# Kernel tuning notes

Hardware: AMD Instinct MI355X
Metric: run time of the kernel (lower is better)

Reference implementation:

```python
import jax, jax.numpy as jnp
import numpy as np

NEG_SLOPE = 0.01  # nn.LeakyReLU default

def leaky_relu(v):
    return jnp.where(v >= 0, v, NEG_SLOPE * v)

def setup_inputs() -> dict:
    key = jax.random.key(0)
    ks = jax.random.split(key, 7)
    B, T, I, H, O = 64, 1024, 512, 1024, 512
    x = jax.random.normal(ks[0], (B, T, I), dtype=jnp.float32)
    # Linear params (stored as [in, out] for x @ W + b)
    W_in = jax.random.normal(ks[1], (I, H), dtype=jnp.float32) * (1.0 / np.sqrt(I))
    b_in = jax.random.normal(ks[2], (H,), dtype=jnp.float32) * 0.01
    W_h = jax.random.normal(ks[3], (2 * H, H), dtype=jnp.float32) * (1.0 / np.sqrt(2 * H))
    b_h = jax.random.normal(ks[4], (H,), dtype=jnp.float32) * 0.01
    W_out = jax.random.normal(ks[5], (H, O), dtype=jnp.float32) * (1.0 / np.sqrt(H))
    b_out = jax.random.normal(ks[6], (O,), dtype=jnp.float32) * 0.01
    return {"x": x, "W_in": W_in, "b_in": b_in, "W_h": W_h, "b_h": b_h,
            "W_out": W_out, "b_out": b_out}

def reference(x, W_in, b_in, W_h, b_h, W_out, b_out):
    B, T, I = x.shape
    H = W_in.shape[1]
    # Precompute input projection for all timesteps in one big GEMM:
    # [B,T,I] @ [I,H] -> [B,T,H], then LeakyReLU.
    h_new_all = leaky_relu(jnp.einsum('bti,ih->bth', x, W_in) + b_in)
    h0 = jnp.zeros((B, H), dtype=x.dtype)

    def step(h, h_new_t):
        combined = jnp.concatenate((h_new_t, h), axis=1)  # [B, 2H]
        h_next = leaky_relu(combined @ W_h + b_h)          # [B, H]
        return h_next, None

    # scan over time axis (sequential dependency on h); dropout_rate=0 => identity
    h_final, _ = jax.lax.scan(step, h0, jnp.swapaxes(h_new_all, 0, 1))
    out = h_final @ W_out + b_out  # [B, O]
    return out
```

## Files before the change

kernel.cpp:

```cpp
#include <hip/hip_runtime.h>
#include <hip/hip_bf16.h>

typedef __attribute__((ext_vector_type(8))) short  s16x8;
typedef __attribute__((ext_vector_type(4))) float  f32x4;
typedef __attribute__((ext_vector_type(4))) unsigned short u16x4;
typedef __attribute__((ext_vector_type(4))) unsigned int   u32x4;

#define B_  64
#define T_  1024
#define I_  512
#define H_  1024
#define O_  512
#define MT_ 65536

#define RG_   8
#define CS_   16

__device__ __forceinline__ unsigned short f2bf(float f) {
    unsigned u = __builtin_bit_cast(unsigned, f);
    u += 0x7FFFu + ((u >> 16) & 1u);
    return (unsigned short)(u >> 16);
}
__device__ __forceinline__ float bf2f(unsigned short h) {
    return __builtin_bit_cast(float, ((unsigned)h) << 16);
}
__device__ __forceinline__ void store_out(float* p, float v) { *p = v; }
__device__ __forceinline__ void store_out(unsigned short* p, float v) { *p = f2bf(v); }
__device__ __forceinline__ void store_nt(float* p, float v) {
    asm volatile("global_store_dword %0, %1, off nt" :: "v"(p), "v"(v) : "memory");
}
__device__ __forceinline__ void store_nt(unsigned short* p, float v) {
    unsigned short h = f2bf(v);
    asm volatile("global_store_short %0, %1, off nt" :: "v"(p), "v"(h) : "memory");
}
__device__ __forceinline__ float to_f32(float v) { return v; }
__device__ __forceinline__ float to_f32(unsigned short v) { return bf2f(v); }

template<typename T> struct pre4;
template<> struct pre4<float>          { using t = f32x4; };
template<> struct pre4<unsigned short> { using t = u16x4; };

__device__ __forceinline__ f32x4 pre_ld(const float* p) {
    f32x4 d; asm volatile("global_load_dwordx4 %0, %1, off nt" : "=v"(d) : "v"(p)); return d;
}
__device__ __forceinline__ u16x4 pre_ld(const unsigned short* p) {
    u16x4 d; asm volatile("global_load_dwordx2 %0, %1, off nt" : "=v"(d) : "v"(p)); return d;
}

#define GL2LDS16(gp, lp) __builtin_amdgcn_global_load_lds( \
    (const __attribute__((address_space(1))) void*)(gp),   \
    (__attribute__((address_space(3))) void*)(lp), 16, 0, 0)

__global__ void cvt_x(const float* __restrict__ src, unsigned short* __restrict__ dst, int n) {
    int stride = gridDim.x * blockDim.x * 4;
    for (int i = (blockIdx.x * blockDim.x + threadIdx.x) * 4; i < n; i += stride) {
        const float4 v = *(const float4*)(src + i);
        u16x4 o;
        o.x = f2bf(v.x); o.y = f2bf(v.y); o.z = f2bf(v.z); o.w = f2bf(v.w);
        *(u16x4*)(dst + i) = o;
    }
}

__global__ void cvt_t(const float* __restrict__ src, unsigned short* __restrict__ dst,
                      int SR, int SC, int row_off) {
    __shared__ unsigned short tile[32][33];
    int c0 = blockIdx.x * 32, r0 = blockIdx.y * 32;
    int tx = threadIdx.x, ty = threadIdx.y;
    #pragma unroll
    for (int i = 0; i < 32; i += 8)
        tile[ty + i][tx] = f2bf(src[(size_t)(row_off + r0 + ty + i) * SC + c0 + tx]);
    __syncthreads();
    #pragma unroll
    for (int i = 0; i < 32; i += 8)
        dst[(size_t)(c0 + ty + i) * SR + r0 + tx] = tile[tx][ty + i];
}

__global__ void strip_h(const unsigned* __restrict__ src, unsigned short* __restrict__ dst) {
    int idx = blockIdx.x * blockDim.x + threadIdx.x;
    u32x4 v = *(const u32x4*)(src + idx * 4);
    int rg = idx >> 11, c2 = idx & 2047;
    int q = c2 >> 9, c3 = c2 & 511;
    int j = c3 >> 6, c = c3 & 63;
    int p = c >> 5, a = (c >> 3) & 3, row = c & 7;
    int grow = rg * 8 + row;
    int col = q * 256 + j * 32 + a * 8 + p * 4;
    u16x4 o;
    o.x = (unsigned short)(v.x >> 16); o.y = (unsigned short)(v.y >> 16);
    o.z = (unsigned short)(v.z >> 16); o.w = (unsigned short)(v.w >> 16);
    *(u16x4*)(dst + (size_t)grow * H_ + col) = o;
}

template<typename OutT, bool LRELU, bool SCATTER>
__global__ __launch_bounds__(256)
void gemm_bf16(const unsigned short* __restrict__ A,
               const unsigned short* __restrict__ BT,
               const float* __restrict__ bias,
               OutT* __restrict__ C, int M, int K, int N)
{
    __shared__ unsigned short As[4096];
    __shared__ unsigned short Bs[4096];
    const int tid = threadIdx.x, lane = tid & 63, wid = tid >> 6;
    const int wr = wid >> 1, wc = wid & 1;
    const int m0 = blockIdx.x * 128, n0 = blockIdx.y * 128;

    f32x4 acc[4][4] = {};

    const int c = wid * 2;
    const int srow = lane >> 2;
    const int scol = (lane & 3) * 8;
    const unsigned short* Ag0 = A  + (size_t)(m0 + c * 16 + srow) * K + scol;
    const unsigned short* Ag1 = A  + (size_t)(m0 + c * 16 + 16 + srow) * K + scol;
    const unsigned short* Bg0 = BT + (size_t)(n0 + c * 16 + srow) * K + scol;
    const unsigned short* Bg1 = BT + (size_t)(n0 + c * 16 + 16 + srow) * K + scol;

    for (int k0 = 0; k0 < K; k0 += 32) {
        __syncthreads();
        GL2LDS16(Ag0 + k0, As + c * 512);
        GL2LDS16(Ag1 + k0, As + (c + 1) * 512);
        GL2LDS16(Bg0 + k0, Bs + c * 512);
        GL2LDS16(Bg1 + k0, Bs + (c + 1) * 512);
        __syncthreads();

        s16x8 af[4], bfr[4];
        #pragma unroll
        for (int i = 0; i < 4; i++)
            af[i] = *(const s16x8*)(As + (wr * 64 + i * 16 + (lane & 15)) * 32 + (lane >> 4) * 8);
        #pragma unroll
        for (int j = 0; j < 4; j++)
            bfr[j] = *(const s16x8*)(Bs + (wc * 64 + j * 16 + (lane & 15)) * 32 + (lane >> 4) * 8);
        #pragma unroll
        for (int i = 0; i < 4; i++)
            #pragma unroll
            for (int j = 0; j < 4; j++)
                acc[i][j] = __builtin_amdgcn_mfma_f32_16x16x32_bf16(af[i], bfr[j], acc[i][j], 0, 0, 0);
    }

    #pragma unroll
    for (int j = 0; j < 4; j++) {
        const int n = n0 + wc * 64 + j * 16 + (lane & 15);
        const float bv = bias[n];
        #pragma unroll
        for (int i = 0; i < 4; i++) {
            #pragma unroll
            for (int r = 0; r < 4; r++) {
                const int m = m0 + wr * 64 + i * 16 + (lane >> 4) * 4 + r;
                if (m < M) {
                    float v = acc[i][j][r] + bv;
                    if (LRELU) v = v >= 0.f ? v : 0.01f * v;
                    if (SCATTER) {
                        size_t row = (size_t)((m & (T_ - 1)) * B_ + (m >> 10));
                        store_nt(&C[row * N + n], v);
                    } else {
                        store_out(&C[(size_t)m * N + n], v);
                    }
                }
            }
        }
    }
}


#define TAGLD2(d, BASE, OFFSTR, SC) asm volatile( \
    "global_load_dwordx4 %0, %1, off offset:" OFFSTR " " SC \
    : "=v"(d) : "v"(BASE))

#define POLLBODY(SC) do { \
    TAGLD2(tv[0],  tA, "0",   SC); TAGLD2(tv[1],  tA, "512",  SC); \
    TAGLD2(tv[2],  tA, "1024",SC); TAGLD2(tv[3],  tA, "1536", SC); \
    TAGLD2(tv[4],  tA, "2048",SC); TAGLD2(tv[5],  tA, "2560", SC); \
    TAGLD2(tv[6],  tA, "3072",SC); TAGLD2(tv[7],  tA, "3584", SC); \
    TAGLD2(tv[8],  tB, "0",   SC); TAGLD2(tv[9],  tB, "512",  SC); \
    TAGLD2(tv[10], tB, "1024",SC); TAGLD2(tv[11], tB, "1536", SC); \
    TAGLD2(tv[12], tB, "2048",SC); TAGLD2(tv[13], tB, "2560", SC); \
    TAGLD2(tv[14], tB, "3072",SC); TAGLD2(tv[15], tB, "3584", SC); \
    } while (0)

#define STEP(S, PVUSE, PVFILL) do { \
    const char* hc32 = (const char*)hbuf32 + (((S) & 1) << 18); \
    char*       hn32 = (char*)hbuf32 + ((((S) + 1) & 1) << 18); \
    const unsigned tagS = (unsigned)(S); \
    const char* tA = hc32 + tbA_off; \
    const char* tB = tA + 4096; \
    float* pb = pbuf + ((S) & 1) * 2176; \
    for (int i_ = 0; i_ < slp; ++i_) __builtin_amdgcn_s_sleep(2); \
    u32x4 tv[16]; \
    unsigned ok = 0u; \
    int rounds_ = 0; \
    for (;;) { \
        if (!ok) { \
            if (!gmode) { POLLBODY("sc0"); } else { POLLBODY("sc0 sc1"); } \
            asm volatile("s_waitcnt vmcnt(0)" ::: "memory"); \
            __builtin_amdgcn_sched_barrier(0); \
            unsigned d_ = 0; \
            _Pragma("unroll") \
            for (int i = 0; i < 16; i++) \
                d_ |= (tv[i].x ^ tagS) | (tv[i].y ^ tagS) | (tv[i].z ^ tagS) | (tv[i].w ^ tagS); \
            ok = ((d_ & 0xFFFFu) == 0u) ? 1u : 0u; \
        } \
        ++rounds_; \
        if (__all((int)ok)) break; \
        if ((rounds_ & 15) == 0) { \
            unsigned fl; \
            asm volatile("global_load_dword %0, %1, off sc0 sc1\n\t" \
                         "s_waitcnt vmcnt(0)" : "=v"(fl) : "v"(dflag) : "memory"); \
            bool anyfl = __any((int)(fl != 0u)); \
            if (!gmode && (anyfl || rounds_ > 96)) { \
                if (!anyfl && lane == 0) { \
                    unsigned one_ = 1u; \
                    asm volatile("global_store_dword %0, %1, off sc0 sc1" \
                                 :: "v"(dflag), "v"(one_) : "memory"); \
                } \
                gmode = 1u; \
                asm volatile("global_store_dwordx4 %0, %1, off sc0 sc1" \
                             :: "v"(lastsp), "v"(lastow) : "memory"); \
            } \
        } \
        __builtin_amdgcn_s_sleep(1); \
    } \
    slp = (rounds_ > 1) ? (slp + 4 > 24 ? 24 : slp + 4) : (slp > 0 ? slp - 1 : 0); \
    { const int sn = ((S) + 1 < T_) ? (S) + 1 : (S); \
      PVFILL = pre_ld(pre + ((size_t)sn * B_ + hrow) * H_ + col0); } \
    f32x4 ac[4] = {}; \
    _Pragma("unroll") \
    for (int cg = 0; cg < 4; ++cg) { \
        const char* pE = wE + cg * 32768; \
        const char* pO = wO + cg * 32768; \
        _Pragma("unroll") \
        for (int j = 0; j < 8; ++j) { \
            u32x4 a2_ = tv[2 * j], b2_ = tv[2 * j + 1]; \
            u32x4 f_; \
            f_.x = (a2_.x >> 16) | (a2_.y & 0xFFFF0000u); \
            f_.y = (a2_.z >> 16) | (a2_.w & 0xFFFF0000u); \
            f_.z = (b2_.x >> 16) | (b2_.y & 0xFFFF0000u); \
            f_.w = (b2_.z >> 16) | (b2_.w & 0xFFFF0000u); \
            s16x8 hfrag = __builtin_bit_cast(s16x8, f_); \
            s16x8 g = *(const s16x8*)(((j & 1) ? pO : pE) + j * 64); \
            ac[cg] = __builtin_amdgcn_mfma_f32_16x16x32_bf16(g, hfrag, ac[cg], 0, 0, 0); \
        } \
    } \
    if (l15 < 8) { \
        float* pw_ = pb + (w * 8 + l15) * 68 + l4 * 4; \
        *(f32x4*)(pw_ +  0) = ac[0]; \
        *(f32x4*)(pw_ + 16) = ac[1]; \
        *(f32x4*)(pw_ + 32) = ac[2]; \
        *(f32x4*)(pw_ + 48) = ac[3]; \
    } \
    asm volatile("s_waitcnt lgkmcnt(0)" ::: "memory"); \
    __builtin_amdgcn_s_barrier(); \
    asm volatile("" ::: "memory"); \
    if (l15 < 8) { \
        const float* pr_ = pb + l15 * 68 + w * 16 + l4 * 4; \
        f32x4 s0 = *(const f32x4*)(pr_); \
        f32x4 s1 = *(const f32x4*)(pr_ + 544); \
        f32x4 s2 = *(const f32x4*)(pr_ + 1088); \
        f32x4 s3 = *(const f32x4*)(pr_ + 1632); \
        f32x4 sm = (s0 + s1) + (s2 + s3); \
        u32x4 ow; \
        _Pragma("unroll") \
        for (int r = 0; r < 4; r++) { \
            float v = sm[r] + to_f32(PVUSE[r]); \
            v = v >= 0.f ? v : 0.01f * v; \
            ow[r] = ((unsigned)f2bf(v) << 16) | (tagS + 1u); \
        } \
        char* sp = hn32 + sp_off; \
        if (!gmode) { \
            asm volatile("global_store_dwordx4 %0, %1, off sc0" \
                         :: "v"(sp), "v"(ow) : "memory"); \
        } else { \
            asm volatile("global_store_dwordx4 %0, %1, off sc0 sc1" \
                         :: "v"(sp), "v"(ow) : "memory"); \
        } \
        lastow = ow; lastsp = sp; \
    } \
  } while (0)

template<typename PreT>
__global__ __launch_bounds__(256, 1)
void rnn_scan19(const unsigned short* __restrict__ WbotT,
                const PreT* __restrict__ pre,
                unsigned* __restrict__ hbuf32,
                unsigned* __restrict__ dflag)
{
    using p4_t = typename pre4<PreT>::t;
    __shared__ unsigned short Ws[64 * 1024];
    __shared__ float pbuf[2 * 2176];
    const int tid = threadIdx.x, lane = tid & 63, w = tid >> 6;
    const int rg = (int)blockIdx.x & 7;
    const int cs = (int)blockIdx.x >> 3;
    const int n0 = cs * 64;

    for (int idx = tid; idx < 64 * 128; idx += 256) {
        int r = idx >> 7, kb = (idx & 127) * 16;
        s16x8 v = *(const s16x8*)(WbotT + (size_t)(n0 + r) * H_ + (idx & 127) * 8);
        *(s16x8*)((char*)Ws + r * 2048 + (kb ^ ((r & 7) << 4))) = v;
    }
    __syncthreads();

    const int l15 = lane & 15, l4 = lane >> 4;
    const int hrow = rg * 8 + (l15 & 7);
    const int col0 = n0 + w * 16 + l4 * 4;

    const int tbA_off = rg * 32768 + w * 8192 + (lane >> 4) * 128 + (lane & 7) * 16;
    const int q_ = col0 >> 8, j_ = (col0 >> 5) & 7, a_ = (col0 >> 3) & 3, p_ = (col0 >> 2) & 1;
    const int sp_off = rg * 32768 + q_ * 8192 + j_ * 1024 + p_ * 512 + (a_ * 8 + (l15 & 7)) * 16;

    const int b6 = (l15 >> 2) & 1;
    const char* wsRow = (const char*)Ws + l15 * 2048 + ((l4 * 16) ^ ((l15 & 3) << 4)) + w * 512;
    const char* wE = wsRow + b6 * 64;
    const char* wO = wsRow - b6 * 64;

    int slp = 0;
    unsigned gmode = 0;
    u32x4 lastow = {};
    char* lastsp = (char*)dflag + 1024 + tid * 16;

    p4_t pvA, pvB;
    pvA = pre_ld(pre + (size_t)hrow * H_ + col0);
    asm volatile("s_waitcnt vmcnt(0)" ::: "memory");

    for (int t = 0; t < T_; t += 2) {
        STEP(t,     pvA, pvB);
        STEP(t + 1, pvB, pvA);
    }
}

extern "C" void kernel_launch(void* const* d_in, const int* in_sizes, int n_in,
                              void* d_out, int out_size, void* d_ws, size_t ws_size,
                              hipStream_t stream)
{
    const float* x     = (const float*)d_in[0];
    const float* W_in  = (const float*)d_in[1];
    const float* b_in  = (const float*)d_in[2];
    const float* W_h   = (const float*)d_in[3];
    const float* b_h   = (const float*)d_in[4];
    const float* W_out = (const float*)d_in[5];
    const float* b_out = (const float*)d_in[6];
    float* out = (float*)d_out;

    char* ws = (char*)d_ws;
    size_t off = 0;
    auto alloc = [&](size_t bytes) { void* p = ws + off; off += (bytes + 255) & ~(size_t)255; return p; };

    unsigned short* Xb    = (unsigned short*)alloc((size_t)MT_ * I_ * 2);
    unsigned short* WinT  = (unsigned short*)alloc((size_t)H_ * I_ * 2);
    unsigned short* WtopT = (unsigned short*)alloc((size_t)H_ * H_ * 2);
    unsigned short* WbotT = (unsigned short*)alloc((size_t)H_ * H_ * 2);
    unsigned short* WoutT = (unsigned short*)alloc((size_t)O_ * H_ * 2);
    unsigned short* Abuf  = (unsigned short*)alloc((size_t)MT_ * H_ * 2);
    unsigned*       hbuf32 = (unsigned*)alloc((size_t)2 * B_ * H_ * 4);
    unsigned*       dbuf  = (unsigned*)alloc(8192);
    unsigned short* hfin  = (unsigned short*)alloc((size_t)B_ * H_ * 2);
    void* pre = ws + off;
    const bool pre_f32 = (off + (size_t)MT_ * H_ * 4) <= ws_size;

    hipMemsetAsync(hbuf32, 0, (size_t)2 * B_ * H_ * 4, stream);
    hipMemsetAsync(dbuf, 0, 8192, stream);

    cvt_x<<<2048, 256, 0, stream>>>(x, Xb, MT_ * I_);
    dim3 tb(32, 8);
    cvt_t<<<dim3(H_ / 32, I_ / 32), tb, 0, stream>>>(W_in,  WinT,  I_, H_, 0);
    cvt_t<<<dim3(H_ / 32, H_ / 32), tb, 0, stream>>>(W_h,   WtopT, H_, H_, 0);
    cvt_t<<<dim3(H_ / 32, H_ / 32), tb, 0, stream>>>(W_h,   WbotT, H_, H_, H_);
    cvt_t<<<dim3(O_ / 32, H_ / 32), tb, 0, stream>>>(W_out, WoutT, H_, O_, 0);

    gemm_bf16<unsigned short, true, false>
        <<<dim3(MT_ / 128, H_ / 128), 256, 0, stream>>>(Xb, WinT, b_in, Abuf, MT_, I_, H_);

    if (pre_f32) {
        gemm_bf16<float, false, true>
            <<<dim3(MT_ / 128, H_ / 128), 256, 0, stream>>>(Abuf, WtopT, b_h, (float*)pre, MT_, H_, H_);
        rnn_scan19<float><<<RG_ * CS_, 256, 0, stream>>>(WbotT, (const float*)pre, hbuf32, dbuf);
    } else {
        gemm_bf16<unsigned short, false, true>
            <<<dim3(MT_ / 128, H_ / 128), 256, 0, stream>>>(Abuf, WtopT, b_h, (unsigned short*)pre, MT_, H_, H_);
        rnn_scan19<unsigned short><<<RG_ * CS_, 256, 0, stream>>>(WbotT, (const unsigned short*)pre, hbuf32, dbuf);
    }

    strip_h<<<64, 256, 0, stream>>>(hbuf32, hfin);
    gemm_bf16<float, false, false>
        <<<dim3(1, O_ / 128), 256, 0, stream>>>(hfin, WoutT, b_out, out, B_, H_, O_);
}
```

Before: 2.875 ms.

## Fuse second projection GEMM into scan kernel with per-element ready tags

Merges the h_new@W_top GEMM into the same launch as the recurrent scan. The first 128 blocks run the scan, and the remaining blocks compute the GEMM in time-chunk order. They write bf16 values packed with a ready tag into a 32-bit buffer, which the scan blocks poll before consuming each timestep. The aim is to overlap the large precompute GEMM with the latency-bound sequential scan instead of running them back to back. In exchange, it adds a full memset of the tagged buffer, coherent (sc0 sc1) stores and loads, spin-waits, and a reliance on the scan blocks being co-resident with the GEMM blocks.

After: 2.744 ms. -4.5%, faster.

```diff
diff --git a/kernel.cpp b/kernel.cpp
--- a/kernel.cpp
+++ b/kernel.cpp
@@ -12,6 +12,7 @@
 #define H_  1024
 #define O_  512
 #define MT_ 65536
+#define G2_ 4096
 
 #define RG_   8
 #define CS_   16
@@ -26,26 +27,6 @@
 }
 __device__ __forceinline__ void store_out(float* p, float v) { *p = v; }
 __device__ __forceinline__ void store_out(unsigned short* p, float v) { *p = f2bf(v); }
-__device__ __forceinline__ void store_nt(float* p, float v) {
-    asm volatile("global_store_dword %0, %1, off nt" :: "v"(p), "v"(v) : "memory");
-}
-__device__ __forceinline__ void store_nt(unsigned short* p, float v) {
-    unsigned short h = f2bf(v);
-    asm volatile("global_store_short %0, %1, off nt" :: "v"(p), "v"(h) : "memory");
-}
-__device__ __forceinline__ float to_f32(float v) { return v; }
-__device__ __forceinline__ float to_f32(unsigned short v) { return bf2f(v); }
-
-template<typename T> struct pre4;
-template<> struct pre4<float>          { using t = f32x4; };
-template<> struct pre4<unsigned short> { using t = u16x4; };
-
-__device__ __forceinline__ f32x4 pre_ld(const float* p) {
-    f32x4 d; asm volatile("global_load_dwordx4 %0, %1, off nt" : "=v"(d) : "v"(p)); return d;
-}
-__device__ __forceinline__ u16x4 pre_ld(const unsigned short* p) {
-    u16x4 d; asm volatile("global_load_dwordx2 %0, %1, off nt" : "=v"(d) : "v"(p)); return d;
-}
 
 #define GL2LDS16(gp, lp) __builtin_amdgcn_global_load_lds( \
     (const __attribute__((address_space(1))) void*)(gp),   \
@@ -90,7 +71,7 @@
     *(u16x4*)(dst + (size_t)grow * H_ + col) = o;
 }
 
-template<typename OutT, bool LRELU, bool SCATTER>
+template<typename OutT, bool LRELU>
 __global__ __launch_bounds__(256)
 void gemm_bf16(const unsigned short* __restrict__ A,
                const unsigned short* __restrict__ BT,
@@ -147,12 +128,7 @@
                 if (m < M) {
                     float v = acc[i][j][r] + bv;
                     if (LRELU) v = v >= 0.f ? v : 0.01f * v;
-                    if (SCATTER) {
-                        size_t row = (size_t)((m & (T_ - 1)) * B_ + (m >> 10));
-                        store_nt(&C[row * N + n], v);
-                    } else {
-                        store_out(&C[(size_t)m * N + n], v);
-                    }
+                    store_out(&C[(size_t)m * N + n], v);
                 }
             }
         }
@@ -174,6 +150,20 @@
     TAGLD2(tv[12], tB, "2048",SC); TAGLD2(tv[13], tB, "2560", SC); \
     TAGLD2(tv[14], tB, "3072",SC); TAGLD2(tv[15], tB, "3584", SC); \
     } while (0)
+
+#define VALPRE(PV, S) do { \
+    unsigned tk = (unsigned)(((PV.x & 0xFFFFu) == 1u) & ((PV.y & 0xFFFFu) == 1u) & \
+                             ((PV.z & 0xFFFFu) == 1u) & ((PV.w & 0xFFFFu) == 1u)); \
+    while (!__all((int)tk)) { \
+        if (!tk) { \
+            const unsigned* pp_ = pre32 + ((size_t)(S) * B_ + hrow) * H_ + col0; \
+            asm volatile("global_load_dwordx4 %0, %1, off sc0 sc1\n\t" \
+                         "s_waitcnt vmcnt(0)" : "=v"(PV) : "v"(pp_) : "memory"); \
+            tk = (unsigned)(((PV.x & 0xFFFFu) == 1u) & ((PV.y & 0xFFFFu) == 1u) & \
+                            ((PV.z & 0xFFFFu) == 1u) & ((PV.w & 0xFFFFu) == 1u)); \
+        } \
+        __builtin_amdgcn_s_sleep(2); \
+    } } while (0)
 
 #define STEP(S, PVUSE, PVFILL) do { \
     const char* hc32 = (const char*)hbuf32 + (((S) & 1) << 18); \
@@ -219,7 +209,8 @@
     } \
     slp = (rounds_ > 1) ? (slp + 4 > 24 ? 24 : slp + 4) : (slp > 0 ? slp - 1 : 0); \
     { const int sn = ((S) + 1 < T_) ? (S) + 1 : (S); \
-      PVFILL = pre_ld(pre + ((size_t)sn * B_ + hrow) * H_ + col0); } \
+      const unsigned* pp_ = pre32 + ((size_t)sn * B_ + hrow) * H_ + col0; \
+      asm volatile("global_load_dwordx4 %0, %1, off sc0 sc1" : "=v"(PVFILL) : "v"(pp_)); } \
     f32x4 ac[4] = {}; \
     _Pragma("unroll") \
     for (int cg = 0; cg < 4; ++cg) { \
@@ -248,6 +239,7 @@
     asm volatile("s_waitcnt lgkmcnt(0)" ::: "memory"); \
     __builtin_amdgcn_s_barrier(); \
     asm volatile("" ::: "memory"); \
+    VALPRE(PVUSE, S); \
     if (l15 < 8) { \
         const float* pr_ = pb + l15 * 68 + w * 16 + l4 * 4; \
         f32x4 s0 = *(const f32x4*)(pr_); \
@@ -258,7 +250,7 @@
         u32x4 ow; \
         _Pragma("unroll") \
         for (int r = 0; r < 4; r++) { \
-            float v = sm[r] + to_f32(PVUSE[r]); \
+            float v = sm[r] + bf2f((unsigned short)(PVUSE[r] >> 16)); \
             v = v >= 0.f ? v : 0.01f * v; \
             ow[r] = ((unsigned)f2bf(v) << 16) | (tagS + 1u); \
         } \
@@ -274,19 +266,81 @@
     } \
   } while (0)
 
-template<typename PreT>
 __global__ __launch_bounds__(256, 1)
-void rnn_scan19(const unsigned short* __restrict__ WbotT,
-                const PreT* __restrict__ pre,
+void gemm2_scan(const unsigned short* __restrict__ Abuf,
+                const unsigned short* __restrict__ WtopT,
+                const float* __restrict__ b_h,
+                const unsigned short* __restrict__ WbotT,
+                unsigned* __restrict__ pre32,
                 unsigned* __restrict__ hbuf32,
                 unsigned* __restrict__ dflag)
 {
-    using p4_t = typename pre4<PreT>::t;
-    __shared__ unsigned short Ws[64 * 1024];
-    __shared__ float pbuf[2 * 2176];
+    __shared__ char smem[148480];
+    const int bid = (int)blockIdx.x;
     const int tid = threadIdx.x, lane = tid & 63, w = tid >> 6;
-    const int rg = (int)blockIdx.x & 7;
-    const int cs = (int)blockIdx.x >> 3;
+
+    if (bid >= 128) {
+        unsigned short* As = (unsigned short*)smem;
+        unsigned short* Bs = As + 4096;
+        const int g = bid - 128;
+        const int tch = g >> 9, b = (g >> 3) & 63, nb = g & 7;
+        const int m0 = b * 1024 + tch * 128, n0 = nb * 128;
+        const int wr = w >> 1, wc = w & 1;
+
+        f32x4 acc[4][4] = {};
+        const int c = w * 2, srow = lane >> 2, scol = (lane & 3) * 8;
+        const unsigned short* Ag0 = Abuf  + (size_t)(m0 + c * 16 + srow) * H_ + scol;
+        const unsigned short* Ag1 = Abuf  + (size_t)(m0 + c * 16 + 16 + srow) * H_ + scol;
+        const unsigned short* Bg0 = WtopT + (size_t)(n0 + c * 16 + srow) * H_ + scol;
+        const unsigned short* Bg1 = WtopT + (size_t)(n0 + c * 16 + 16 + srow) * H_ + scol;
+
+        for (int k0 = 0; k0 < H_; k0 += 32) {
+            __syncthreads();
+            GL2LDS16(Ag0 + k0, As + c * 512);
+            GL2LDS16(Ag1 + k0, As + (c + 1) * 512);
+            GL2LDS16(Bg0 + k0, Bs + c * 512);
+            GL2LDS16(Bg1 + k0, Bs + (c + 1) * 512);
+            __syncthreads();
+
+            s16x8 af[4], bfr[4];
+            #pragma unroll
+            for (int i = 0; i < 4; i++)
+                af[i] = *(const s16x8*)(As + (wr * 64 + i * 16 + (lane & 15)) * 32 + (lane >> 4) * 8);
+            #pragma unroll
+            for (int j = 0; j < 4; j++)
+                bfr[j] = *(const s16x8*)(Bs + (wc * 64 + j * 16 + (lane & 15)) * 32 + (lane >> 4) * 8);
+            #pragma unroll
+            for (int i = 0; i < 4; i++)
+                #pragma unroll
+                for (int j = 0; j < 4; j++)
+                    acc[i][j] = __builtin_amdgcn_mfma_f32_16x16x32_bf16(af[i], bfr[j], acc[i][j], 0, 0, 0);
+        }
+
+        #pragma unroll
+        for (int j = 0; j < 4; j++) {
+            const int n = n0 + wc * 64 + j * 16 + (lane & 15);
+            const float bv = b_h[n];
+            #pragma unroll
+            for (int i = 0; i < 4; i++) {
+                #pragma unroll
+                for (int r = 0; r < 4; r++) {
+                    const int m = m0 + wr * 64 + i * 16 + (lane >> 4) * 4 + r;
+                    float v = acc[i][j][r] + bv;
+                    size_t row = (size_t)((m & (T_ - 1)) * B_ + (m >> 10));
+                    unsigned ow = ((unsigned)f2bf(v) << 16) | 1u;
+                    unsigned* p = pre32 + row * H_ + n;
+                    asm volatile("global_store_dword %0, %1, off sc0 sc1"
+                                 :: "v"(p), "v"(ow) : "memory");
+                }
+            }
+        }
+        return;
+    }
+
+    unsigned short* Ws = (unsigned short*)smem;
+    float* pbuf = (float*)(smem + 131072);
+    const int rg = bid & 7;
+    const int cs = bid >> 3;
     const int n0 = cs * 64;
 
     for (int idx = tid; idx < 64 * 128; idx += 256) {
@@ -314,9 +368,10 @@
     u32x4 lastow = {};
     char* lastsp = (char*)dflag + 1024 + tid * 16;
 
-    p4_t pvA, pvB;
-    pvA = pre_ld(pre + (size_t)hrow * H_ + col0);
-    asm volatile("s_waitcnt vmcnt(0)" ::: "memory");
+    u32x4 pvA, pvB;
+    {   const unsigned* pp_ = pre32 + (size_t)hrow * H_ + col0;
+        asm volatile("global_load_dwordx4 %0, %1, off sc0 sc1" : "=v"(pvA) : "v"(pp_));
+        asm volatile("s_waitcnt vmcnt(0)" ::: "memory"); }
 
     for (int t = 0; t < T_; t += 2) {
         STEP(t,     pvA, pvB);
@@ -350,11 +405,11 @@
     unsigned*       hbuf32 = (unsigned*)alloc((size_t)2 * B_ * H_ * 4);
     unsigned*       dbuf  = (unsigned*)alloc(8192);
     unsigned short* hfin  = (unsigned short*)alloc((size_t)B_ * H_ * 2);
-    void* pre = ws + off;
-    const bool pre_f32 = (off + (size_t)MT_ * H_ * 4) <= ws_size;
+    unsigned*       pre32 = (unsigned*)alloc((size_t)MT_ * H_ * 4);
 
     hipMemsetAsync(hbuf32, 0, (size_t)2 * B_ * H_ * 4, stream);
     hipMemsetAsync(dbuf, 0, 8192, stream);
+    hipMemsetAsync(pre32, 0, (size_t)MT_ * H_ * 4, stream);
 
     cvt_x<<<2048, 256, 0, stream>>>(x, Xb, MT_ * I_);
     dim3 tb(32, 8);
@@ -363,20 +418,12 @@
     cvt_t<<<dim3(H_ / 32, H_ / 32), tb, 0, stream>>>(W_h,   WbotT, H_, H_, H_);
     cvt_t<<<dim3(O_ / 32, H_ / 32), tb, 0, stream>>>(W_out, WoutT, H_, O_, 0);
 
-    gemm_bf16<unsigned short, true, false>
+    gemm_bf16<unsigned short, true>
         <<<dim3(MT_ / 128, H_ / 128), 256, 0, stream>>>(Xb, WinT, b_in, Abuf, MT_, I_, H_);
 
-    if (pre_f32) {
-        gemm_bf16<float, false, true>
-            <<<dim3(MT_ / 128, H_ / 128), 256, 0, stream>>>(Abuf, WtopT, b_h, (float*)pre, MT_, H_, H_);
-        rnn_scan19<float><<<RG_ * CS_, 256, 0, stream>>>(WbotT, (const float*)pre, hbuf32, dbuf);
-    } else {
-        gemm_bf16<unsigned short, false, true>
-            <<<dim3(MT_ / 128, H_ / 128), 256, 0, stream>>>(Abuf, WtopT, b_h, (unsigned short*)pre, MT_, H_, H_);
-        rnn_scan19<unsigned short><<<RG_ * CS_, 256, 0, stream>>>(WbotT, (const unsigned short*)pre, hbuf32, dbuf);
-    }
+    gemm2_scan<<<128 + G2_, 256, 0, stream>>>(Abuf, WtopT, b_h, WbotT, pre32, hbuf32, dbuf);
 
     strip_h<<<64, 256, 0, stream>>>(hbuf32, hfin);
-    gemm_bf16<float, false, false>
+    gemm_bf16<float, false>
         <<<dim3(1, O_ / 128), 256, 0, stream>>>(hfin, WoutT, b_out, out, B_, H_, O_);
 }
```
